# Performance work log

Measured on AMD Instinct MI355X. Metric: run time of the kernel, lower is better.

The kernel has to match this reference:

```python
import jax, jax.numpy as jnp
import numpy as np

BN_EPS = 1e-5

def setup_inputs() -> dict:
    key = jax.random.key(0)
    ks = jax.random.split(key, 7)
    B, C_IN, C_P, N = 4, 256, 128, 4096
    sc_in = 1.0 / np.sqrt(C_IN)
    sc_p = 1.0 / np.sqrt(C_P)
    return {
        "x": jax.random.normal(ks[0], (B, C_IN, N), dtype=jnp.float32),
        "Wt": jax.random.normal(ks[1], (C_P, C_IN), dtype=jnp.float32) * sc_in,
        "Wp": jax.random.normal(ks[2], (C_P, C_IN), dtype=jnp.float32) * sc_in,
        "Wg": jax.random.normal(ks[3], (C_P, C_IN), dtype=jnp.float32) * sc_in,
        "Wz": jax.random.normal(ks[4], (C_IN, C_P), dtype=jnp.float32) * sc_p,
        "gamma": jnp.ones((C_IN,), dtype=jnp.float32),
        "beta": jnp.zeros((C_IN,), dtype=jnp.float32),
    }

def reference(x, Wt, Wp, Wg, Wz, gamma, beta):
    # x: [B, C_in, N]; 1x1 Conv1d == channel matmul
    t = jnp.einsum('oc,bcn->bon', Wt, x)   # [B, Cp, N]
    p = jnp.einsum('oc,bcn->bon', Wp, x)   # [B, Cp, N]
    g = jnp.einsum('oc,bcn->bon', Wg, x)   # [B, Cp, N]
    # att = bmm(t^T, p): [B, N, N]; softmax over dim=1 (non-standard axis)
    att = jnp.einsum('bcn,bcm->bnm', t, p)
    att = jax.nn.softmax(att, axis=1)
    # y = bmm(att, g^T): [B, N, Cp] -> permute to [B, Cp, N]
    y = jnp.einsum('bnm,bcm->bcn', att, g)
    z = jnp.einsum('oc,bcn->bon', Wz, y)   # [B, C_in, N]
    # BatchNorm1d (training-mode batch stats over batch+spatial)
    mean = jnp.mean(z, axis=(0, 2), keepdims=True)
    var = jnp.var(z, axis=(0, 2), keepdims=True)
    z_hat = (z - mean) * jax.lax.rsqrt(var + BN_EPS)
    out = z_hat * gamma[None, :, None] + beta[None, :, None] + x
    return out
```

## Files before the change

### kernel.cpp

```cpp
#include <hip/hip_runtime.h>
#include <hip/hip_fp16.h>

#define B_SZ 4
#define CIN  256
#define CP   128
#define NN   4096
#define NT   32
#define KSL  4

typedef _Float16 half_t;
typedef _Float16 f16x8 __attribute__((ext_vector_type(8)));
typedef float f32x4 __attribute__((ext_vector_type(4)));

#define GPTR(p) ((const __attribute__((address_space(1))) void*)(p))
#define LPTR(p) ((__attribute__((address_space(3))) void*)(p))

__device__ __forceinline__ float wave_sum64(float v){
  #pragma unroll
  for (int o = 32; o > 0; o >>= 1) v += __shfl_xor(v, o, 64);
  return v;
}

__global__ __launch_bounds__(256) void split_w(
    const float* __restrict__ Wt, const float* __restrict__ Wp,
    const float* __restrict__ Wg, half_t* __restrict__ Wh,
    half_t* __restrict__ Wl)
{
  const int sel = blockIdx.x;
  const float* W = (sel == 0) ? Wt : ((sel == 1) ? Wp : Wg);
  half_t* oh = Wh + sel * (CP * CIN);
  half_t* ol = Wl + sel * (CP * CIN);
  #pragma unroll
  for (int i = 0; i < 8; ++i){
    int i4 = blockIdx.y * 2048 + threadIdx.x + i * 256;
    float4 v = ((const float4*)W)[i4];
    v.x *= 16.f; v.y *= 16.f; v.z *= 16.f; v.w *= 16.f;
    union { half_t h[4]; uint2 u; } hh, ll;
    hh.h[0] = (half_t)v.x; ll.h[0] = (half_t)(v.x - (float)hh.h[0]);
    hh.h[1] = (half_t)v.y; ll.h[1] = (half_t)(v.y - (float)hh.h[1]);
    hh.h[2] = (half_t)v.z; ll.h[2] = (half_t)(v.z - (float)hh.h[2]);
    hh.h[3] = (half_t)v.w; ll.h[3] = (half_t)(v.w - (float)hh.h[3]);
    *(uint2*)(oh + i4 * 4) = hh.u;
    *(uint2*)(ol + i4 * 4) = ll.u;
  }
}

__global__ __launch_bounds__(256) void split_x(
    const float* __restrict__ x, half_t* __restrict__ xTh,
    half_t* __restrict__ xTl)
{
  const int b  = blockIdx.z;
  const int c0 = blockIdx.y * 64;
  const int n0 = blockIdx.x * 64;
  __shared__ float lds[64][68];
  const int tid = threadIdx.x;
  #pragma unroll
  for (int i = 0; i < 4; ++i){
    int idx = tid + i * 256;
    int cr = idx >> 4, nq = idx & 15;
    float4 v = *(const float4*)(x + ((size_t)b * CIN + c0 + cr) * NN + n0 + nq * 4);
    *(float4*)&lds[cr][nq * 4] = v;
  }
  __syncthreads();
  #pragma unroll
  for (int i = 0; i < 8; ++i){
    int idx = tid + i * 256;
    int nl = idx >> 5;
    int cp = (idx & 31) * 2;
    float v0 = lds[cp][nl], v1 = lds[cp + 1][nl];
    half_t h0 = (half_t)v0, h1 = (half_t)v1;
    half_t l0 = (half_t)(v0 - (float)h0), l1 = (half_t)(v1 - (float)h1);
    union { half_t h[2]; unsigned int u; } ph, pl;
    ph.h[0] = h0; ph.h[1] = h1;
    pl.h[0] = l0; pl.h[1] = l1;
    size_t o = ((size_t)b * NN + n0 + nl) * CIN + c0 + cp;
    *(unsigned int*)(xTh + o) = ph.u;
    *(unsigned int*)(xTl + o) = pl.u;
  }
}

__global__ __launch_bounds__(256) void tpg_gemm(
    const half_t* __restrict__ Wh, const half_t* __restrict__ Wl,
    const half_t* __restrict__ xTh, const half_t* __restrict__ xTl,
    half_t* __restrict__ tTh, half_t* __restrict__ tTl,
    half_t* __restrict__ pTh, half_t* __restrict__ pTl,
    half_t* __restrict__ gF)
{
  const int b   = blockIdx.z;
  const int sel = blockIdx.y;
  const int n0  = blockIdx.x * 64;
  const half_t* Ah_g = Wh + sel * (CP * CIN);
  const half_t* Al_g = Wl + sel * (CP * CIN);
  const half_t* Bh_g = xTh + ((size_t)b * NN + n0) * CIN;
  const half_t* Bl_g = xTl + ((size_t)b * NN + n0) * CIN;

  __shared__ half_t lds[24576];
  const int tid = threadIdx.x;
  const int wid = tid >> 6, lane = tid & 63;
  const int wo = wid >> 1, wn = wid & 1;
  const int lr = lane & 15, lq = lane >> 4;

  f32x4 acc[4][2];
  #pragma unroll
  for (int i = 0; i < 4; ++i)
    #pragma unroll
    for (int j = 0; j < 2; ++j) acc[i][j] = (f32x4){0.f,0.f,0.f,0.f};

  #pragma unroll 1
  for (int kc = 0; kc < CIN; kc += 64){
    #pragma unroll
    for (int it = 0; it < 4; ++it){
      int seg = wid * 4 + it;
      int row = seg * 8 + (lane >> 3);
      int us  = (lane & 7) ^ (row & 7);
      size_t go = (size_t)row * CIN + kc + us * 8;
      __builtin_amdgcn_global_load_lds(GPTR(Ah_g + go), LPTR(lds + seg*512), 16, 0, 0);
      __builtin_amdgcn_global_load_lds(GPTR(Al_g + go), LPTR(lds + 8192 + seg*512), 16, 0, 0);
    }
    #pragma unroll
    for (int it = 0; it < 2; ++it){
      int seg = wid * 2 + it;
      int row = seg * 8 + (lane >> 3);
      int us  = (lane & 7) ^ (row & 7);
      size_t go = (size_t)row * CIN + kc + us * 8;
      __builtin_amdgcn_global_load_lds(GPTR(Bh_g + go), LPTR(lds + 16384 + seg*512), 16, 0, 0);
      __builtin_amdgcn_global_load_lds(GPTR(Bl_g + go), LPTR(lds + 20480 + seg*512), 16, 0, 0);
    }
    asm volatile("s_waitcnt vmcnt(0)" ::: "memory");
    __syncthreads();

    #pragma unroll
    for (int kk = 0; kk < 2; ++kk){
      f16x8 ah[4], al4[4], bh[2], bl[2];
      #pragma unroll
      for (int f = 0; f < 4; ++f){
        int rA = wo * 64 + f * 16 + lr;
        int cA = (kk*32 + lq*8) ^ ((rA & 7) * 8);
        ah[f]  = *(const f16x8*)(lds + rA * 64 + cA);
        al4[f] = *(const f16x8*)(lds + 8192 + rA * 64 + cA);
      }
      #pragma unroll
      for (int f = 0; f < 2; ++f){
        int rB = wn * 32 + f * 16 + lr;
        int cB = (kk*32 + lq*8) ^ ((rB & 7) * 8);
        bh[f] = *(const f16x8*)(lds + 16384 + rB * 64 + cB);
        bl[f] = *(const f16x8*)(lds + 20480 + rB * 64 + cB);
      }
      #pragma unroll
      for (int fo = 0; fo < 4; ++fo)
        #pragma unroll
        for (int fn = 0; fn < 2; ++fn){
          acc[fo][fn] = __builtin_amdgcn_mfma_f32_16x16x32_f16(ah[fo],  bh[fn], acc[fo][fn], 0,0,0);
          acc[fo][fn] = __builtin_amdgcn_mfma_f32_16x16x32_f16(al4[fo], bh[fn], acc[fo][fn], 0,0,0);
          acc[fo][fn] = __builtin_amdgcn_mfma_f32_16x16x32_f16(ah[fo],  bl[fn], acc[fo][fn], 0,0,0);
        }
    }
    __syncthreads();
  }

  if (sel < 2){
    half_t* Ohi = ((sel == 0) ? tTh : pTh) + (size_t)b * NN * CP;
    half_t* Olo = ((sel == 0) ? tTl : pTl) + (size_t)b * NN * CP;
    float (*ldsT)[132] = (float (*)[132])lds;
    #pragma unroll
    for (int fo = 0; fo < 4; ++fo)
      #pragma unroll
      for (int fn = 0; fn < 2; ++fn)
        #pragma unroll
        for (int r = 0; r < 4; ++r){
          int n = wn * 32 + fn * 16 + lr;
          int o = wo * 64 + fo * 16 + lq * 4 + r;
          ldsT[n][o] = acc[fo][fn][r] * 0.0625f;
        }
    __syncthreads();
    #pragma unroll
    for (int it = 0; it < 16; ++it){
      int idx = tid + it * 256;
      int nl = idx >> 6;
      int cp = (idx & 63) * 2;
      float v0 = ldsT[nl][cp], v1 = ldsT[nl][cp + 1];
      half_t h0 = (half_t)v0, h1 = (half_t)v1;
      half_t l0 = (half_t)(v0 - (float)h0), l1 = (half_t)(v1 - (float)h1);
      union { half_t h[2]; unsigned int u; } ph, pl;
      ph.h[0] = h0; ph.h[1] = h1;
      pl.h[0] = l0; pl.h[1] = l1;
      *(unsigned int*)(Ohi + (size_t)(n0 + nl) * CP + cp) = ph.u;
      *(unsigned int*)(Olo + (size_t)(n0 + nl) * CP + cp) = pl.u;
    }
  } else {
    half_t* G = gF + (size_t)b * CP * NN;
    #pragma unroll
    for (int fo = 0; fo < 4; ++fo)
      #pragma unroll
      for (int r = 0; r < 4; ++r){
        int o = wo * 64 + fo * 16 + lq * 4 + r;
        #pragma unroll
        for (int fn = 0; fn < 2; ++fn){
          int n = n0 + wn * 32 + fn * 16 + lr;
          G[(size_t)o * NN + n] = (half_t)(acc[fo][fn][r] * 0.0625f);
        }
      }
  }
}

__global__ __launch_bounds__(256) void s_gemm(
    const half_t* __restrict__ tTh, const half_t* __restrict__ tTl,
    const half_t* __restrict__ pTh, const half_t* __restrict__ pTl,
    half_t* __restrict__ ST, float* __restrict__ pmax,
    float* __restrict__ psum)
{
  const int b  = blockIdx.z;
  const int m0 = blockIdx.x * 128;
  const int n0 = blockIdx.y * 128;
  const size_t tb = (size_t)b * NN * CP;
  half_t* STb = ST + (size_t)b * NN * NN;
  __shared__ half_t lds[4 * 128 * 64];
  const int tid = threadIdx.x;
  const int wid = tid >> 6, lane = tid & 63;
  const int wn = wid >> 1, wm = wid & 1;
  const int lr = lane & 15, lq = lane >> 4;

  f32x4 acc[4][4];
  #pragma unroll
  for (int i = 0; i < 4; ++i)
    #pragma unroll
    for (int j = 0; j < 4; ++j) acc[i][j] = (f32x4){0.f,0.f,0.f,0.f};

  const half_t* baseA_h = tTh + tb + (size_t)n0 * CP;
  const half_t* baseA_l = tTl + tb + (size_t)n0 * CP;
  const half_t* baseB_h = pTh + tb + (size_t)m0 * CP;
  const half_t* baseB_l = pTl + tb + (size_t)m0 * CP;

  #pragma unroll 1
  for (int kc = 0; kc < CP; kc += 64){
    #pragma unroll
    for (int it = 0; it < 4; ++it){
      int seg = wid * 4 + it;
      int row = seg * 8 + (lane >> 3);
      int us  = (lane & 7) ^ (row & 7);
      size_t go = (size_t)row * CP + kc + us * 8;
      __builtin_amdgcn_global_load_lds(GPTR(baseA_h + go), LPTR(lds + seg*512), 16, 0, 0);
      __builtin_amdgcn_global_load_lds(GPTR(baseA_l + go), LPTR(lds + 8192 + seg*512), 16, 0, 0);
      __builtin_amdgcn_global_load_lds(GPTR(baseB_h + go), LPTR(lds + 16384 + seg*512), 16, 0, 0);
      __builtin_amdgcn_global_load_lds(GPTR(baseB_l + go), LPTR(lds + 24576 + seg*512), 16, 0, 0);
    }
    asm volatile("s_waitcnt vmcnt(0)" ::: "memory");
    __syncthreads();

    #pragma unroll
    for (int kk = 0; kk < 2; ++kk){
      f16x8 ah[4], al[4], bh[4], bl[4];
      #pragma unroll
      for (int f = 0; f < 4; ++f){
        int rA = wn*64 + f*16 + lr;
        int cA = (kk*32 + lq*8) ^ ((rA & 7) * 8);
        ah[f] = *(const f16x8*)(lds + rA*64 + cA);
        al[f] = *(const f16x8*)(lds + 8192 + rA*64 + cA);
        int rB = wm*64 + f*16 + lr;
        int cB = (kk*32 + lq*8) ^ ((rB & 7) * 8);
        bh[f] = *(const f16x8*)(lds + 16384 + rB*64 + cB);
        bl[f] = *(const f16x8*)(lds + 24576 + rB*64 + cB);
      }
      #pragma unroll
      for (int fn = 0; fn < 4; ++fn)
        #pragma unroll
        for (int fm = 0; fm < 4; ++fm){
          acc[fn][fm] = __builtin_amdgcn_mfma_f32_16x16x32_f16(ah[fn], bh[fm], acc[fn][fm], 0,0,0);
          acc[fn][fm] = __builtin_amdgcn_mfma_f32_16x16x32_f16(al[fn], bh[fm], acc[fn][fm], 0,0,0);
          acc[fn][fm] = __builtin_amdgcn_mfma_f32_16x16x32_f16(ah[fn], bl[fm], acc[fn][fm], 0,0,0);
        }
    }
    __syncthreads();
  }

  float* red  = (float*)lds;
  float* red2 = (float*)lds + 256;

  float cmax[4];
  #pragma unroll
  for (int fm = 0; fm < 4; ++fm){
    float t = -3.0e38f;
    #pragma unroll
    for (int fn = 0; fn < 4; ++fn)
      #pragma unroll
      for (int r = 0; r < 4; ++r) t = fmaxf(t, acc[fn][fm][r]);
    t = fmaxf(t, __shfl_xor(t, 16, 64));
    t = fmaxf(t, __shfl_xor(t, 32, 64));
    cmax[fm] = t;
  }
  if (lq == 0){
    #pragma unroll
    for (int fm = 0; fm < 4; ++fm) red[(wid*4+fm)*16 + lr] = cmax[fm];
  }
  __syncthreads();
  #pragma unroll
  for (int fm = 0; fm < 4; ++fm)
    cmax[fm] = fmaxf(red[((wm)*4+fm)*16 + lr], red[((2+wm)*4+fm)*16 + lr]);

  float csum[4] = {0.f, 0.f, 0.f, 0.f};
  #pragma unroll
  for (int fn = 0; fn < 4; ++fn)
    #pragma unroll
    for (int r = 0; r < 4; ++r){
      int n = n0 + wn*64 + fn*16 + lq*4 + r;
      half_t* dst = STb + (size_t)n * NN + m0 + wm*64;
      #pragma unroll
      for (int fm = 0; fm < 4; ++fm){
        float e = __expf(acc[fn][fm][r] - cmax[fm]);
        csum[fm] += e;
        dst[fm*16 + lr] = (half_t)e;
      }
    }
  #pragma unroll
  for (int fm = 0; fm < 4; ++fm){
    csum[fm] += __shfl_xor(csum[fm], 16, 64);
    csum[fm] += __shfl_xor(csum[fm], 32, 64);
  }
  __syncthreads();
  if (lq == 0){
    #pragma unroll
    for (int fm = 0; fm < 4; ++fm) red2[(wid*4+fm)*16 + lr] = csum[fm];
  }
  __syncthreads();
  if (wn == 0 && lq == 0){
    #pragma unroll
    for (int fm = 0; fm < 4; ++fm){
      int m = m0 + wm*64 + fm*16 + lr;
      pmax[((size_t)b * NT + blockIdx.y) * NN + m] = cmax[fm];
      psum[((size_t)b * NT + blockIdx.y) * NN + m] = red2[((wm)*4+fm)*16 + lr]
                                                   + red2[((2+wm)*4+fm)*16 + lr];
    }
  }
}

__global__ __launch_bounds__(256) void merge_corr(
    const float* __restrict__ pmax, const float* __restrict__ psum,
    float* __restrict__ corr)
{
  const size_t base = (size_t)blockIdx.y * NT * NN;
  const int m = blockIdx.x * 256 + threadIdx.x;
  float pm[NT];
  float mx = -3.0e38f;
  #pragma unroll
  for (int nt = 0; nt < NT; ++nt){
    pm[nt] = pmax[base + (size_t)nt * NN + m];
    mx = fmaxf(mx, pm[nt]);
  }
  float den = 0.f;
  #pragma unroll
  for (int nt = 0; nt < NT; ++nt){
    pm[nt] = __expf(pm[nt] - mx);
    den += psum[base + (size_t)nt * NN + m] * pm[nt];
  }
  const float r = 1.f / den;
  #pragma unroll
  for (int nt = 0; nt < NT; ++nt)
    corr[base + (size_t)nt * NN + m] = pm[nt] * r;
}

__global__ __launch_bounds__(256) void y_gemm(
    const half_t* __restrict__ gF, const half_t* __restrict__ ST,
    const float* __restrict__ corr, float* __restrict__ yp)
{
  const int b  = blockIdx.z;
  const int n0 = blockIdx.x * 64;
  const int nt = blockIdx.x >> 1;
  const int ks = blockIdx.y;
  const half_t* G   = gF + (size_t)b * CP * NN;
  const half_t* STb = ST + (size_t)b * NN * NN;
  const float* corb = corr + ((size_t)b * NT + nt) * NN;
  __shared__ half_t As[128*64];
  __shared__ half_t Bs[64*64];
  const int tid = threadIdx.x;
  const int wid = tid >> 6, lane = tid & 63;
  const int wc = wid >> 1, wn = wid & 1;
  const int lr = lane & 15, lq = lane >> 4;

  f32x4 acc[4][2];
  #pragma unroll
  for (int i = 0; i < 4; ++i)
    #pragma unroll
    for (int j = 0; j < 2; ++j) acc[i][j] = (f32x4){0.f,0.f,0.f,0.f};

  #pragma unroll 1
  for (int st = 0; st < 16; ++st){
    const int mc = ks * (NN / KSL) + st * 64;
    #pragma unroll
    for (int it = 0; it < 4; ++it){
      int seg = wid * 4 + it;
      int row = seg * 8 + (lane >> 3);
      int us  = (lane & 7) ^ (row & 7);
      __builtin_amdgcn_global_load_lds(GPTR(G + (size_t)row * NN + mc + us*8),
                                       LPTR(As + seg*512), 16, 0, 0);
    }
    #pragma unroll
    for (int i = 0; i < 4; ++i){
      int idx = tid + i * 256;
      int r = idx >> 4;
      int q = idx & 15;
      int mm = mc + q * 4;
      union { half_t h[4]; uint2 u2; } ev, eo;
      ev.u2 = *(const uint2*)(STb + (size_t)(n0 + r) * NN + mm);
      float4 cr = *(const float4*)(corb + mm);
      eo.h[0] = (half_t)((float)ev.h[0] * cr.x);
      eo.h[1] = (half_t)((float)ev.h[1] * cr.y);
      eo.h[2] = (half_t)((float)ev.h[2] * cr.z);
      eo.h[3] = (half_t)((float)ev.h[3] * cr.w);
      int c4 = (q * 4) ^ ((r & 7) * 8);
      *(uint2*)(Bs + r * 64 + c4) = eo.u2;
    }
    asm volatile("s_waitcnt vmcnt(0)" ::: "memory");
    __syncthreads();

    #pragma unroll
    for (int kk = 0; kk < 2; ++kk){
      f16x8 af[4], bf[2];
      #pragma unroll
      for (int f = 0; f < 4; ++f){
        int rA = wc*64 + f*16 + lr;
        af[f] = *(const f16x8*)(As + rA*64 + ((kk*32 + lq*8) ^ ((rA & 7)*8)));
      }
      #pragma unroll
      for (int f = 0; f < 2; ++f){
        int rB = wn*32 + f*16 + lr;
        bf[f] = *(const f16x8*)(Bs + rB*64 + ((kk*32 + lq*8) ^ ((rB & 7)*8)));
      }
      #pragma unroll
      for (int fc = 0; fc < 4; ++fc)
        #pragma unroll
        for (int fn = 0; fn < 2; ++fn)
          acc[fc][fn] = __builtin_amdgcn_mfma_f32_16x16x32_f16(af[fc], bf[fn], acc[fc][fn], 0,0,0);
    }
    __syncthreads();
  }
  #pragma unroll
  for (int fc = 0; fc < 4; ++fc)
    #pragma unroll
    for (int r = 0; r < 4; ++r){
      int c = wc*64 + fc*16 + lq*4 + r;
      float* dst = yp + (((size_t)b * KSL + ks) * CP + c) * NN + n0;
      #pragma unroll
      for (int fn = 0; fn < 2; ++fn) dst[wn*32 + fn*16 + lr] = acc[fc][fn][r];
    }
}

__global__ __launch_bounds__(256) void z_gemm(
    const float* __restrict__ Wz, const float* __restrict__ yp,
    float* __restrict__ z)
{
  const int b  = blockIdx.z;
  const int o0 = blockIdx.y * 128;
  const int n0 = blockIdx.x * 64;
  const float* y0 = yp + ((size_t)b * KSL + 0) * CP * NN;
  const float* y1 = yp + ((size_t)b * KSL + 1) * CP * NN;
  const float* y2 = yp + ((size_t)b * KSL + 2) * CP * NN;
  const float* y3 = yp + ((size_t)b * KSL + 3) * CP * NN;
  float* zb = z + (size_t)b * CIN * NN;

  __shared__ float a_s[32][132];
  __shared__ float b_s[32][64];

  const int tid = threadIdx.x;
  const int tx = tid & 15, ty = tid >> 4;

  float acc[2][4][4];
  #pragma unroll
  for (int qa = 0; qa < 2; ++qa)
    #pragma unroll
    for (int i = 0; i < 4; ++i)
      #pragma unroll
      for (int j = 0; j < 4; ++j) acc[qa][i][j] = 0.f;

  for (int k0 = 0; k0 < CP; k0 += 32){
    #pragma unroll
    for (int i = 0; i < 4; ++i){
      int f4i = tid + i * 256;
      int c  = f4i >> 3;
      int k4 = f4i & 7;
      float4 w = *(const float4*)(Wz + (size_t)(o0 + c) * CP + k0 + k4 * 4);
      a_s[k4*4+0][c] = w.x;
      a_s[k4*4+1][c] = w.y;
      a_s[k4*4+2][c] = w.z;
      a_s[k4*4+3][c] = w.w;
    }
    #pragma unroll
    for (int i = 0; i < 2; ++i){
      int f4i = tid + i * 256;
      int kk = f4i >> 4;
      int n4 = f4i & 15;
      const size_t off = (size_t)(k0 + kk) * NN + n0 + n4 * 4;
      float4 v0 = *(const float4*)(y0 + off);
      float4 v1 = *(const float4*)(y1 + off);
      float4 v2 = *(const float4*)(y2 + off);
      float4 v3 = *(const float4*)(y3 + off);
      float4 sv;
      sv.x = v0.x + v1.x + v2.x + v3.x;
      sv.y = v0.y + v1.y + v2.y + v3.y;
      sv.z = v0.z + v1.z + v2.z + v3.z;
      sv.w = v0.w + v1.w + v2.w + v3.w;
      *(float4*)&b_s[kk][n4*4] = sv;
    }
    __syncthreads();
    #pragma unroll
    for (int kk = 0; kk < 32; ++kk){
      float af[8], bf[4];
      *(float4*)&af[0] = *(const float4*)&a_s[kk][ty*4];
      *(float4*)&af[4] = *(const float4*)&a_s[kk][ty*4+64];
      *(float4*)&bf[0] = *(const float4*)&b_s[kk][tx*4];
      #pragma unroll
      for (int qa = 0; qa < 2; ++qa)
        #pragma unroll
        for (int i = 0; i < 4; ++i)
          #pragma unroll
          for (int j = 0; j < 4; ++j)
            acc[qa][i][j] = fmaf(af[qa*4+i], bf[j], acc[qa][i][j]);
    }
    __syncthreads();
  }
  #pragma unroll
  for (int qa = 0; qa < 2; ++qa)
    #pragma unroll
    for (int i = 0; i < 4; ++i){
      const int row = o0 + qa*64 + ty*4 + i;
      float4 v = make_float4(acc[qa][i][0], acc[qa][i][1],
                             acc[qa][i][2], acc[qa][i][3]);
      *(float4*)(zb + (size_t)row * NN + n0 + tx*4) = v;
    }
}

__global__ __launch_bounds__(256) void bn_stats(
    const float* __restrict__ z, float* __restrict__ mean,
    float* __restrict__ rstd)
{
  const int c = blockIdx.x;
  const int tid = threadIdx.x;
  float s = 0.f, s2 = 0.f;
  for (int b = 0; b < B_SZ; ++b){
    const float4* row = (const float4*)(z + ((size_t)b * CIN + c) * NN);
    #pragma unroll
    for (int i = 0; i < 4; ++i){
      float4 v = row[tid + i*256];
      s  += v.x + v.y + v.z + v.w;
      s2 += v.x*v.x + v.y*v.y + v.z*v.z + v.w*v.w;
    }
  }
  s  = wave_sum64(s);
  s2 = wave_sum64(s2);
  __shared__ float rs[4];
  __shared__ float rq[4];
  const int wid = tid >> 6, lane = tid & 63;
  if (lane == 0){ rs[wid] = s; rq[wid] = s2; }
  __syncthreads();
  if (tid == 0){
    const float S1 = rs[0]+rs[1]+rs[2]+rs[3];
    const float S2 = rq[0]+rq[1]+rq[2]+rq[3];
    const float inv = 1.f / (float)(B_SZ * NN);
    const float m = S1 * inv;
    const float var = S2 * inv - m * m;
    mean[c] = m;
    rstd[c] = 1.f / sqrtf(var + 1e-5f);
  }
}

__global__ __launch_bounds__(256) void finalize_k(
    const float* __restrict__ z, const float* __restrict__ x,
    const float* __restrict__ mean, const float* __restrict__ rstd,
    const float* __restrict__ gamma, const float* __restrict__ beta,
    float* __restrict__ out)
{
  const int total = B_SZ * CIN * NN / 4;
  for (int i = blockIdx.x * blockDim.x + threadIdx.x; i < total;
       i += gridDim.x * blockDim.x){
    const int c = (i >> 10) & (CIN - 1);
    float4 zv = ((const float4*)z)[i];
    float4 xv = ((const float4*)x)[i];
    const float m = mean[c], r = rstd[c], ga = gamma[c], be = beta[c];
    float4 o;
    o.x = (zv.x - m) * r * ga + be + xv.x;
    o.y = (zv.y - m) * r * ga + be + xv.y;
    o.z = (zv.z - m) * r * ga + be + xv.z;
    o.w = (zv.w - m) * r * ga + be + xv.w;
    ((float4*)out)[i] = o;
  }
}

extern "C" void kernel_launch(void* const* d_in, const int* in_sizes, int n_in,
                              void* d_out, int out_size, void* d_ws, size_t ws_size,
                              hipStream_t stream)
{
  const float* x     = (const float*)d_in[0];
  const float* Wt    = (const float*)d_in[1];
  const float* Wp    = (const float*)d_in[2];
  const float* Wg    = (const float*)d_in[3];
  const float* Wz    = (const float*)d_in[4];
  const float* gamma = (const float*)d_in[5];
  const float* beta  = (const float*)d_in[6];
  float* out = (float*)d_out;

  float* wsf = (float*)d_ws;
  size_t off = 0;
  half_t* ST  = (half_t*)(wsf + off); off += (size_t)B_SZ * NN * NN / 2;
  half_t* tTh = (half_t*)(wsf + off); off += (size_t)B_SZ*NN*CP/2;
  half_t* tTl = (half_t*)(wsf + off); off += (size_t)B_SZ*NN*CP/2;
  half_t* pTh = (half_t*)(wsf + off); off += (size_t)B_SZ*NN*CP/2;
  half_t* pTl = (half_t*)(wsf + off); off += (size_t)B_SZ*NN*CP/2;
  half_t* gF  = (half_t*)(wsf + off); off += (size_t)B_SZ*CP*NN/2;
  half_t* xTh = (half_t*)(wsf + off); off += (size_t)B_SZ*NN*CIN/2;
  half_t* xTl = (half_t*)(wsf + off); off += (size_t)B_SZ*NN*CIN/2;
  half_t* Wh  = (half_t*)(wsf + off); off += (size_t)3*CP*CIN/2;
  half_t* Wl  = (half_t*)(wsf + off); off += (size_t)3*CP*CIN/2;
  float*  yp  = wsf + off; off += (size_t)B_SZ * KSL * CP * NN;
  float*  pmax= wsf + off; off += (size_t)B_SZ * NT * NN;
  float*  psum= wsf + off; off += (size_t)B_SZ * NT * NN;
  float*  corr= wsf + off; off += (size_t)B_SZ * NT * NN;
  float*  meanb = wsf + off; off += CIN;
  float*  rstdb = wsf + off; off += CIN;
  float*  z = (float*)ST;

  split_w <<<dim3(3, 4),           256, 0, stream>>>(Wt, Wp, Wg, Wh, Wl);
  split_x <<<dim3(64, 4, B_SZ),    256, 0, stream>>>(x, xTh, xTl);
  tpg_gemm<<<dim3(64, 3, B_SZ),    256, 0, stream>>>(Wh, Wl, xTh, xTl,
                                                     tTh, tTl, pTh, pTl, gF);
  s_gemm    <<<dim3(32, 32, B_SZ), 256, 0, stream>>>(tTh, tTl, pTh, pTl,
                                                     ST, pmax, psum);
  merge_corr<<<dim3(16, B_SZ),     256, 0, stream>>>(pmax, psum, corr);
  y_gemm    <<<dim3(64, KSL, B_SZ),256, 0, stream>>>(gF, ST, corr, yp);
  z_gemm    <<<dim3(64, 2, B_SZ),  256, 0, stream>>>(Wz, yp, z);
  bn_stats  <<<dim3(CIN),          256, 0, stream>>>(z, meanb, rstdb);
  finalize_k<<<dim3(2048),         256, 0, stream>>>(z, x, meanb, rstdb,
                                                     gamma, beta, out);
}
```

Baseline: 252.7 us.

## Stage softmax tile in LDS for coalesced stores, remap blocks across XCDs, prefetch y_gemm

s_gemm now writes the exponentiated score tile into padded LDS and then copies it to global memory as contiguous 16-byte rows, replacing scattered 2-byte stores. Both s_gemm and y_gemm use a remapped 1D grid that interleaves blocks modulo 8, aiming for locality on each XCD's L2. y_gemm software-pipelines the ST/corr register loads one step ahead with double-buffered registers, so global latency overlaps the MFMA work. The cost is more register pressure and LDS reuse of the staging buffer.

```diff
diff --git a/kernel.cpp b/kernel.cpp
--- a/kernel.cpp
+++ b/kernel.cpp
@@ -210,8 +210,11 @@
     float* __restrict__ psum)
 {
   const int b  = blockIdx.z;
-  const int m0 = blockIdx.x * 128;
-  const int n0 = blockIdx.y * 128;
+  const int bx = blockIdx.x;
+  const int tile  = (bx & 7) * 128 + (bx >> 3);
+  const int ntile = tile >> 5;
+  const int m0 = (tile & 31) * 128;
+  const int n0 = ntile * 128;
   const size_t tb = (size_t)b * NN * CP;
   half_t* STb = ST + (size_t)b * NN * NN;
   __shared__ half_t lds[4 * 128 * 64];
@@ -273,8 +276,9 @@
     __syncthreads();
   }
 
-  float* red  = (float*)lds;
-  float* red2 = (float*)lds + 256;
+  float*  red  = (float*)lds;
+  float*  red2 = (float*)lds + 256;
+  half_t* Eb   = lds + 2048;
 
   float cmax[4];
   #pragma unroll
@@ -302,13 +306,13 @@
   for (int fn = 0; fn < 4; ++fn)
     #pragma unroll
     for (int r = 0; r < 4; ++r){
-      int n = n0 + wn*64 + fn*16 + lq*4 + r;
-      half_t* dst = STb + (size_t)n * NN + m0 + wm*64;
+      int nl = wn*64 + fn*16 + lq*4 + r;
+      half_t* db = Eb + nl*132 + wm*64;
       #pragma unroll
       for (int fm = 0; fm < 4; ++fm){
         float e = __expf(acc[fn][fm][r] - cmax[fm]);
         csum[fm] += e;
-        dst[fm*16 + lr] = (half_t)e;
+        db[fm*16 + lr] = (half_t)e;
       }
     }
   #pragma unroll
@@ -316,19 +320,27 @@
     csum[fm] += __shfl_xor(csum[fm], 16, 64);
     csum[fm] += __shfl_xor(csum[fm], 32, 64);
   }
+  if (lq == 0){
+    #pragma unroll
+    for (int fm = 0; fm < 4; ++fm) red2[(wid*4+fm)*16 + lr] = csum[fm];
+  }
   __syncthreads();
-  if (lq == 0){
-    #pragma unroll
-    for (int fm = 0; fm < 4; ++fm) red2[(wid*4+fm)*16 + lr] = csum[fm];
-  }
-  __syncthreads();
+
+  #pragma unroll
+  for (int it = 0; it < 8; ++it){
+    int idx = tid + it * 256;
+    int row = idx >> 4;
+    int ch  = idx & 15;
+    uint4 v = *(const uint4*)(Eb + row*132 + ch*8);
+    *(uint4*)(STb + (size_t)(n0 + row) * NN + m0 + ch*8) = v;
+  }
   if (wn == 0 && lq == 0){
     #pragma unroll
     for (int fm = 0; fm < 4; ++fm){
       int m = m0 + wm*64 + fm*16 + lr;
-      pmax[((size_t)b * NT + blockIdx.y) * NN + m] = cmax[fm];
-      psum[((size_t)b * NT + blockIdx.y) * NN + m] = red2[((wm)*4+fm)*16 + lr]
-                                                   + red2[((2+wm)*4+fm)*16 + lr];
+      pmax[((size_t)b * NT + ntile) * NN + m] = cmax[fm];
+      psum[((size_t)b * NT + ntile) * NN + m] = red2[((wm)*4+fm)*16 + lr]
+                                              + red2[((2+wm)*4+fm)*16 + lr];
     }
   }
 }
@@ -362,10 +374,14 @@
     const half_t* __restrict__ gF, const half_t* __restrict__ ST,
     const float* __restrict__ corr, float* __restrict__ yp)
 {
-  const int b  = blockIdx.z;
-  const int n0 = blockIdx.x * 64;
-  const int nt = blockIdx.x >> 1;
-  const int ks = blockIdx.y;
+  const int bx  = blockIdx.x;
+  const int lin = (bx & 7) * 128 + (bx >> 3);
+  const int b   = lin >> 8;
+  const int rem = lin & 255;
+  const int ks  = rem >> 6;
+  const int nx  = rem & 63;
+  const int n0  = nx * 64;
+  const int nt  = nx >> 1;
   const half_t* G   = gF + (size_t)b * CP * NN;
   const half_t* STb = ST + (size_t)b * NN * NN;
   const float* corb = corr + ((size_t)b * NT + nt) * NN;
@@ -382,57 +398,92 @@
     #pragma unroll
     for (int j = 0; j < 2; ++j) acc[i][j] = (f32x4){0.f,0.f,0.f,0.f};
 
-  #pragma unroll 1
-  for (int st = 0; st < 16; ++st){
-    const int mc = ks * (NN / KSL) + st * 64;
-    #pragma unroll
-    for (int it = 0; it < 4; ++it){
-      int seg = wid * 4 + it;
-      int row = seg * 8 + (lane >> 3);
-      int us  = (lane & 7) ^ (row & 7);
-      __builtin_amdgcn_global_load_lds(GPTR(G + (size_t)row * NN + mc + us*8),
-                                       LPTR(As + seg*512), 16, 0, 0);
-    }
+  uint2 evA[4]; float4 crA[4];
+  uint2 evB[4]; float4 crB[4];
+
+  {
+    const int mc = ks * (NN / KSL);
     #pragma unroll
     for (int i = 0; i < 4; ++i){
       int idx = tid + i * 256;
-      int r = idx >> 4;
-      int q = idx & 15;
+      int r = idx >> 4, q = idx & 15;
       int mm = mc + q * 4;
-      union { half_t h[4]; uint2 u2; } ev, eo;
-      ev.u2 = *(const uint2*)(STb + (size_t)(n0 + r) * NN + mm);
-      float4 cr = *(const float4*)(corb + mm);
-      eo.h[0] = (half_t)((float)ev.h[0] * cr.x);
-      eo.h[1] = (half_t)((float)ev.h[1] * cr.y);
-      eo.h[2] = (half_t)((float)ev.h[2] * cr.z);
-      eo.h[3] = (half_t)((float)ev.h[3] * cr.w);
-      int c4 = (q * 4) ^ ((r & 7) * 8);
-      *(uint2*)(Bs + r * 64 + c4) = eo.u2;
-    }
-    asm volatile("s_waitcnt vmcnt(0)" ::: "memory");
-    __syncthreads();
-
-    #pragma unroll
-    for (int kk = 0; kk < 2; ++kk){
-      f16x8 af[4], bf[2];
-      #pragma unroll
-      for (int f = 0; f < 4; ++f){
-        int rA = wc*64 + f*16 + lr;
-        af[f] = *(const f16x8*)(As + rA*64 + ((kk*32 + lq*8) ^ ((rA & 7)*8)));
-      }
-      #pragma unroll
-      for (int f = 0; f < 2; ++f){
-        int rB = wn*32 + f*16 + lr;
-        bf[f] = *(const f16x8*)(Bs + rB*64 + ((kk*32 + lq*8) ^ ((rB & 7)*8)));
-      }
-      #pragma unroll
-      for (int fc = 0; fc < 4; ++fc)
-        #pragma unroll
-        for (int fn = 0; fn < 2; ++fn)
-          acc[fc][fn] = __builtin_amdgcn_mfma_f32_16x16x32_f16(af[fc], bf[fn], acc[fc][fn], 0,0,0);
-    }
-    __syncthreads();
-  }
+      evA[i] = *(const uint2*)(STb + (size_t)(n0 + r) * NN + mm);
+      crA[i] = *(const float4*)(corb + mm);
+    }
+  }
+
+#define Y_STEP(ST_IDX, CEV, CCR, NEV, NCR)                                     \
+  {                                                                            \
+    const int st = (ST_IDX);                                                   \
+    const int mc = ks * (NN / KSL) + st * 64;                                  \
+    _Pragma("unroll")                                                          \
+    for (int it = 0; it < 4; ++it){                                            \
+      int seg = wid * 4 + it;                                                  \
+      int row = seg * 8 + (lane >> 3);                                         \
+      int us  = (lane & 7) ^ (row & 7);                                        \
+      __builtin_amdgcn_global_load_lds(GPTR(G + (size_t)row * NN + mc + us*8), \
+                                       LPTR(As + seg*512), 16, 0, 0);          \
+    }                                                                          \
+    _Pragma("unroll")                                                          \
+    for (int i = 0; i < 4; ++i){                                               \
+      int idx = tid + i * 256;                                                 \
+      int r = idx >> 4;                                                        \
+      int q = idx & 15;                                                        \
+      union { half_t h[4]; uint2 u2; } ev, eo;                                 \
+      ev.u2 = CEV[i];                                                          \
+      float4 cr = CCR[i];                                                      \
+      eo.h[0] = (half_t)((float)ev.h[0] * cr.x);                               \
+      eo.h[1] = (half_t)((float)ev.h[1] * cr.y);                               \
+      eo.h[2] = (half_t)((float)ev.h[2] * cr.z);                               \
+      eo.h[3] = (half_t)((float)ev.h[3] * cr.w);                               \
+      int c4 = (q * 4) ^ ((r & 7) * 8);                                        \
+      *(uint2*)(Bs + r * 64 + c4) = eo.u2;                                     \
+    }                                                                          \
+    asm volatile("s_waitcnt vmcnt(0)" ::: "memory");                           \
+    __syncthreads();                                                           \
+    {                                                                          \
+      const int pst = (st < 15) ? st + 1 : 15;                                 \
+      const int pmc = ks * (NN / KSL) + pst * 64;                              \
+      _Pragma("unroll")                                                        \
+      for (int i = 0; i < 4; ++i){                                             \
+        int idx = tid + i * 256;                                               \
+        int r = idx >> 4, q = idx & 15;                                        \
+        int mm = pmc + q * 4;                                                  \
+        NEV[i] = *(const uint2*)(STb + (size_t)(n0 + r) * NN + mm);            \
+        NCR[i] = *(const float4*)(corb + mm);                                  \
+      }                                                                        \
+    }                                                                          \
+    _Pragma("unroll")                                                          \
+    for (int kk = 0; kk < 2; ++kk){                                            \
+      f16x8 af[4], bf[2];                                                      \
+      _Pragma("unroll")                                                        \
+      for (int f = 0; f < 4; ++f){                                             \
+        int rA = wc*64 + f*16 + lr;                                            \
+        af[f] = *(const f16x8*)(As + rA*64 + ((kk*32 + lq*8) ^ ((rA & 7)*8))); \
+      }                                                                        \
+      _Pragma("unroll")                                                        \
+      for (int f = 0; f < 2; ++f){                                             \
+        int rB = wn*32 + f*16 + lr;                                            \
+        bf[f] = *(const f16x8*)(Bs + rB*64 + ((kk*32 + lq*8) ^ ((rB & 7)*8))); \
+      }                                                                        \
+      _Pragma("unroll")                                                        \
+      for (int fc = 0; fc < 4; ++fc)                                           \
+        _Pragma("unroll")                                                      \
+        for (int fn = 0; fn < 2; ++fn)                                         \
+          acc[fc][fn] = __builtin_amdgcn_mfma_f32_16x16x32_f16(                \
+              af[fc], bf[fn], acc[fc][fn], 0,0,0);                             \
+    }                                                                          \
+    __syncthreads();                                                           \
+  }
+
+  #pragma unroll 1
+  for (int sp = 0; sp < 8; ++sp){
+    Y_STEP(2*sp,     evA, crA, evB, crB)
+    Y_STEP(2*sp + 1, evB, crB, evA, crA)
+  }
+#undef Y_STEP
+
   #pragma unroll
   for (int fc = 0; fc < 4; ++fc)
     #pragma unroll
@@ -621,10 +672,10 @@
   split_x <<<dim3(64, 4, B_SZ),    256, 0, stream>>>(x, xTh, xTl);
   tpg_gemm<<<dim3(64, 3, B_SZ),    256, 0, stream>>>(Wh, Wl, xTh, xTl,
                                                      tTh, tTl, pTh, pTl, gF);
-  s_gemm    <<<dim3(32, 32, B_SZ), 256, 0, stream>>>(tTh, tTl, pTh, pTl,
+  s_gemm    <<<dim3(1024, 1, B_SZ),256, 0, stream>>>(tTh, tTl, pTh, pTl,
                                                      ST, pmax, psum);
   merge_corr<<<dim3(16, B_SZ),     256, 0, stream>>>(pmax, psum, corr);
-  y_gemm    <<<dim3(64, KSL, B_SZ),256, 0, stream>>>(gF, ST, corr, yp);
+  y_gemm    <<<dim3(1024),         256, 0, stream>>>(gF, ST, corr, yp);
   z_gemm    <<<dim3(64, 2, B_SZ),  256, 0, stream>>>(Wz, yp, z);
   bn_stats  <<<dim3(CIN),          256, 0, stream>>>(z, meanb, rstdb);
   finalize_k<<<dim3(2048),         256, 0, stream>>>(z, x, meanb, rstdb,
```

New measurement: 274.9 us. +8.8%, slower.
